# Performance work log

Measured on AMD Instinct MI355X. Metric: run time of the kernel, lower is better.

## Reference

```python
import jax, jax.numpy as jnp
import numpy as np


def setup_inputs() -> dict:
    key = jax.random.key(0)
    ks = jax.random.split(key, 12)
    B, N, Dv, E, H, V, T = 128, 196, 512, 512, 1024, 10000, 20
    s = 0.02  # small init scale for numerical stability
    f = lambda k, shp: (jax.random.normal(k, shp, jnp.float32) * s)
    return {
        "features": jax.random.normal(ks[0], (B, N, Dv), jnp.float32),
        "captions": jax.random.randint(ks[1], (B, T), 0, V),
        "W_init_h": f(ks[2], (H, Dv)),
        "W_init_c": f(ks[3], (H, Dv)),
        "W_attn_v": f(ks[4], (1, Dv)),
        "b_attn_v": jnp.zeros((1,), jnp.float32),
        "W_attn_h": f(ks[5], (1, H)),
        "b_attn_h": jnp.zeros((1,), jnp.float32),
        "embed_table": f(ks[6], (V, E)),
        "W_ih": f(ks[7], (4 * H, Dv + E)),
        "W_hh": f(ks[8], (4 * H, H)),
        "b_ih": jnp.zeros((4 * H,), jnp.float32),
        "b_hh": jnp.zeros((4 * H,), jnp.float32),
        "W_out": f(ks[9], (V, H)),
        "b_out": jnp.zeros((V,), jnp.float32),
    }


def reference(features, captions, W_init_h, W_init_c, W_attn_v, b_attn_v,
              W_attn_h, b_attn_h, embed_table, W_ih, W_hh, b_ih, b_hh,
              W_out, b_out):
    B, N, Dv = features.shape
    # _init_hidden: mean over vis_num of linear projections (division by vis_num)
    h0 = jnp.sum(jnp.einsum('bnd,hd->bnh', features, W_init_h), axis=1) / N
    c0 = jnp.sum(jnp.einsum('bnd,hd->bnh', features, W_init_c), axis=1) / N

    emb = embed_table[captions]                      # B,T,E
    emb_t_major = jnp.swapaxes(emb, 0, 1)            # T,B,E
    # visual attention logits are time-invariant; precompute once
    att_v = jnp.einsum('bnd,od->bno', features, W_attn_v) + b_attn_v  # B,N,1

    def step(carry, emb_t):
        h, c = carry
        # soft attention over vis_num locations
        att_h = (h @ W_attn_h.T + b_attn_h)[:, None, :]   # B,1,1
        alpha = jax.nn.softmax(att_v + att_h, axis=1)     # B,N,1
        ctx = jnp.sum(features * alpha, axis=1)           # B,Dv
        # single-step LSTM (PyTorch gate order: i, f, g, o)
        x = jnp.concatenate([ctx, emb_t], axis=-1)        # B,Dv+E
        gates = x @ W_ih.T + h @ W_hh.T + b_ih + b_hh     # B,4H
        i, fg, g, o = jnp.split(gates, 4, axis=-1)
        c_new = jax.nn.sigmoid(fg) * c + jax.nn.sigmoid(i) * jnp.tanh(g)
        h_new = jax.nn.sigmoid(o) * jnp.tanh(c_new)
        words = h_new @ W_out.T + b_out                   # B,V
        return (h_new, c_new), words

    _, word_space = jax.lax.scan(step, (h0, c0), emb_t_major)  # T,B,V
    # pack_padded_sequence with all-equal lengths flattens time-major -> (T*B, V)
    packed = word_space.reshape(-1, word_space.shape[-1])
    return jax.nn.log_softmax(packed, axis=1), jax.nn.softmax(packed, axis=1)
```

## Files before the change

kernel.cpp:

```cpp
#include <hip/hip_runtime.h>
#include <math.h>

#define B    128
#define NLOC 196
#define DV   512
#define EMB  512
#define HD   1024
#define VV   10000
#define TT   20
#define G4   4096
#define VPAD 10112
#define BH   (B*HD)

typedef short bf16x8 __attribute__((ext_vector_type(8)));
typedef float f32x4  __attribute__((ext_vector_type(4)));

__device__ __forceinline__ unsigned short f2bf(float x) {
    unsigned u = __builtin_bit_cast(unsigned, x);
    unsigned r = (u + 0x7fffu + ((u >> 16) & 1u)) >> 16;
    return (unsigned short)r;
}
__device__ __forceinline__ float bf2f(short s) {
    unsigned u = ((unsigned)(unsigned short)s) << 16;
    return __builtin_bit_cast(float, u);
}

__device__ __forceinline__ void gload_lds16(const void* g, void* lds) {
    __builtin_amdgcn_global_load_lds(
        (const __attribute__((address_space(1))) void*)g,
        (__attribute__((address_space(3))) void*)lds, 16, 0, 0);
}


__global__ void fmean_kernel(const float* __restrict__ feat, short* __restrict__ fmean_b) {
    int idx = blockIdx.x * blockDim.x + threadIdx.x;
    if (idx >= B * DV) return;
    int b = idx / DV, d = idx % DV;
    const float* p = feat + (size_t)b * NLOC * DV + d;
    float s = 0.f;
    for (int n = 0; n < NLOC; ++n) s += p[(size_t)n * DV];
    fmean_b[idx] = (short)f2bf(s * (1.0f / NLOC));
}

__global__ void attv_kernel(const float* __restrict__ feat, const float* __restrict__ wv,
                            const float* __restrict__ bv, float* __restrict__ attv) {
    int row  = blockIdx.x;
    int lane = threadIdx.x;
    const float* p = feat + (size_t)row * DV;
    float s = 0.f;
    for (int k = lane; k < DV; k += 64) s += p[k] * wv[k];
    for (int off = 32; off > 0; off >>= 1) s += __shfl_down(s, off);
    if (lane == 0) attv[row] = s + bv[0];
}

__global__ void alpha_kernel(const float* __restrict__ attv, float* __restrict__ alpha) {
    int b   = blockIdx.x;
    int tid = threadIdx.x;
    __shared__ float red[256];
    float v = (tid < NLOC) ? attv[b * NLOC + tid] : -1e30f;
    red[tid] = v; __syncthreads();
    for (int s = 128; s > 0; s >>= 1) { if (tid < s) red[tid] = fmaxf(red[tid], red[tid + s]); __syncthreads(); }
    float m = red[0]; __syncthreads();
    float e = (tid < NLOC) ? expf(v - m) : 0.f;
    red[tid] = e; __syncthreads();
    for (int s = 128; s > 0; s >>= 1) { if (tid < s) red[tid] += red[tid + s]; __syncthreads(); }
    float sum = red[0];
    if (tid < NLOC) alpha[b * NLOC + tid] = e / sum;
}

__global__ void ctx_kernel(const float* __restrict__ feat, const float* __restrict__ alpha,
                           short* __restrict__ ctx_b) {
    int idx = blockIdx.x * blockDim.x + threadIdx.x;
    if (idx >= B * DV) return;
    int b = idx / DV, d = idx % DV;
    const float* p = feat + (size_t)b * NLOC * DV + d;
    const float* a = alpha + b * NLOC;
    float s = 0.f;
    for (int n = 0; n < NLOC; ++n) s += a[n] * p[(size_t)n * DV];
    ctx_b[idx] = (short)f2bf(s);
}

__global__ void emb_gather_kernel(const int* __restrict__ captions, const float* __restrict__ table,
                                  short* __restrict__ emb_b) {
    size_t idx = (size_t)blockIdx.x * blockDim.x + threadIdx.x;
    if (idx >= (size_t)TT * B * EMB) return;
    int k = (int)(idx % EMB);
    int r = (int)(idx / EMB);
    int t = r / B, b = r % B;
    int cap = captions[b * TT + t];
    emb_b[idx] = (short)f2bf(table[(size_t)cap * EMB + k]);
}

__global__ void f2bf_pad_kernel(const float* __restrict__ in, short* __restrict__ out,
                                size_t n, size_t npad) {
    size_t i = (size_t)blockIdx.x * blockDim.x + threadIdx.x;
    if (i >= npad) return;
    out[i] = (i < n) ? (short)f2bf(in[i]) : (short)0;
}

__global__ void whh_perm_kernel(const float* __restrict__ in, short* __restrict__ out) {
    size_t idx = (size_t)blockIdx.x * blockDim.x + threadIdx.x;
    if (idx >= (size_t)G4 * HD) return;
    int k = (int)(idx & (HD - 1));
    int P = (int)(idx >> 10);
    int u = P >> 2, g = P & 3;
    out[idx] = (short)f2bf(in[(size_t)(g * HD + u) * HD + k]);
}

__global__ void hcvt_kernel(const float* __restrict__ h, short* __restrict__ h_bf) {
    int idx = blockIdx.x * blockDim.x + threadIdx.x;
    if (idx >= B * HD) return;
    h_bf[idx] = (short)f2bf(h[idx]);
}

template<int BN, int WR, int WC, bool BF16OUT>
__global__ __launch_bounds__(256)
void gemm_bf16(const short* __restrict__ A, const short* __restrict__ Bw,
               void* __restrict__ C,
               const float* __restrict__ bias0, const float* __restrict__ bias1,
               int NY, int M, int N, int K, int lda, int ldb, int ldc) {
    constexpr int BM = 128;
    constexpr int BK = 32;
    constexpr int WM = BM / WR;
    constexpr int WN = BN / WC;
    constexpr int FM = WM / 16;
    constexpr int FN = WN / 16;
    __shared__ __align__(16) short As[BM * BK];
    __shared__ __align__(16) short Bs[BN * BK];
    const int tid  = threadIdx.x;
    const int wave = tid >> 6, lane = tid & 63;
    const int wr = wave / WC, wc = wave % WC;

    const int nwg = gridDim.x;
    const int qq = nwg >> 3, rr8 = nwg & 7;
    const int p = blockIdx.x;
    const int xcd = p & 7, slot = p >> 3;
    const int lwg = (xcd < rr8) ? (xcd * (qq + 1) + slot)
                                : (rr8 * (qq + 1) + (xcd - rr8) * qq + slot);
    const int m0 = (lwg % NY) * BM;
    const int n0 = (lwg / NY) * BN;
    const int laneoff = lane * 16;

    f32x4 acc[FM][FN] = {};

    for (int k0 = 0; k0 < K; k0 += BK) {
        #pragma unroll
        for (int r = 0; r < 2; ++r) {
            int o   = r * 4096 + wave * 1024 + laneoff;
            int row = o >> 6;
            int gr  = (o >> 4) & 3;
            int col = ((gr ^ ((row >> 1) & 3)) << 3);
            gload_lds16(A + (size_t)(m0 + row) * lda + k0 + col,
                        (char*)As + r * 4096 + wave * 1024);
        }
        constexpr int BBYTES = BN * BK * 2;
        if constexpr (BBYTES >= 4096) {
            #pragma unroll
            for (int r = 0; r < BBYTES / 4096; ++r) {
                int o   = r * 4096 + wave * 1024 + laneoff;
                int row = o >> 6;
                int gr  = (o >> 4) & 3;
                int col = ((gr ^ ((row >> 1) & 3)) << 3);
                gload_lds16(Bw + (size_t)(n0 + row) * ldb + k0 + col,
                            (char*)Bs + r * 4096 + wave * 1024);
            }
        } else {
            constexpr int NW = BBYTES / 1024;
            if (wave < NW) {
                int o   = wave * 1024 + laneoff;
                int row = o >> 6;
                int gr  = (o >> 4) & 3;
                int col = ((gr ^ ((row >> 1) & 3)) << 3);
                gload_lds16(Bw + (size_t)(n0 + row) * ldb + k0 + col,
                            (char*)Bs + wave * 1024);
            }
        }
        __syncthreads();

        bf16x8 a[FM], b[FN];
        const int kfrg = lane >> 4;
        #pragma unroll
        for (int i = 0; i < FM; ++i) {
            int row = wr * WM + i * 16 + (lane & 15);
            a[i] = *(const bf16x8*)&As[row * BK + ((kfrg ^ ((row >> 1) & 3)) << 3)];
        }
        #pragma unroll
        for (int j = 0; j < FN; ++j) {
            int row = wc * WN + j * 16 + (lane & 15);
            b[j] = *(const bf16x8*)&Bs[row * BK + ((kfrg ^ ((row >> 1) & 3)) << 3)];
        }
        #pragma unroll
        for (int i = 0; i < FM; ++i)
            #pragma unroll
            for (int j = 0; j < FN; ++j)
                acc[i][j] = __builtin_amdgcn_mfma_f32_16x16x32_bf16(a[i], b[j], acc[i][j], 0, 0, 0);
        __syncthreads();
    }

    #pragma unroll
    for (int i = 0; i < FM; ++i) {
        #pragma unroll
        for (int j = 0; j < FN; ++j) {
            int col = n0 + wc * WN + j * 16 + (lane & 15);
            if (col >= N) continue;
            float bv = (bias0 ? bias0[col] : 0.f) + (bias1 ? bias1[col] : 0.f);
            #pragma unroll
            for (int q = 0; q < 4; ++q) {
                int row = m0 + wr * WM + i * 16 + (lane >> 4) * 4 + q;
                if (row < M) {
                    float v = acc[i][j][q] + bv;
                    if constexpr (BF16OUT)
                        ((short*)C)[(size_t)row * ldc + col] = (short)f2bf(v);
                    else
                        ((float*)C)[(size_t)row * ldc + col] = v;
                }
            }
        }
    }
}

__global__ __launch_bounds__(256)
void lstm_step6(const short* __restrict__ Hprev, const short* __restrict__ Whh_p,
                const short* __restrict__ pre_t, const short* __restrict__ gctx_b,
                float* __restrict__ cbuf, short* __restrict__ Hnext,
                short* __restrict__ Hall_t) {
    __shared__ __align__(16) short As[64 * 512];
    __shared__ __align__(16) short Ws[32 * 512];
    __shared__ float gsm[4][64][8];
    const int tid  = threadIdx.x;
    const int lane = tid & 63, wave = tid >> 6;
    const int n0 = blockIdx.x * 32;
    const int m0 = blockIdx.y * 64;

    const int arowL = wave * 16 + (lane & 15);
    const int brow0 = lane & 15;
    const int brow1 = 16 + (lane & 15);
    const int kg    = lane >> 4;

    f32x4 acc0 = {}, acc1 = {};

    for (int h2 = 0; h2 < 2; ++h2) {
        const int k0 = h2 * 512;
        #pragma unroll
        for (int it = 0; it < 16; ++it) {
            int fg  = it * 256 + tid;
            int row = fg >> 6;
            int g   = fg & 63;
            int col = (g ^ (row & 7)) * 8;
            gload_lds16(Hprev + (size_t)(m0 + row) * HD + k0 + col,
                        (char*)As + it * 4096 + wave * 1024);
        }
        #pragma unroll
        for (int it = 0; it < 8; ++it) {
            int fg  = it * 256 + tid;
            int row = fg >> 6;
            int g   = fg & 63;
            int col = (g ^ (row & 7)) * 8;
            gload_lds16(Whh_p + (size_t)(n0 + row) * HD + k0 + col,
                        (char*)Ws + it * 4096 + wave * 1024);
        }
        __syncthreads();
        #pragma unroll
        for (int ks = 0; ks < 16; ++ks) {
            int lg = ks * 4 + kg;
            bf16x8 a  = *(const bf16x8*)((const char*)As + arowL * 1024 + ((lg ^ (arowL & 7)) << 4));
            bf16x8 w0 = *(const bf16x8*)((const char*)Ws + brow0 * 1024 + ((lg ^ (brow0 & 7)) << 4));
            bf16x8 w1 = *(const bf16x8*)((const char*)Ws + brow1 * 1024 + ((lg ^ (brow1 & 7)) << 4));
            acc0 = __builtin_amdgcn_mfma_f32_16x16x32_bf16(a, w0, acc0, 0, 0, 0);
            acc1 = __builtin_amdgcn_mfma_f32_16x16x32_bf16(a, w1, acc1, 0, 0, 0);
        }
        __syncthreads();
    }

    #pragma unroll
    for (int q = 0; q < 4; ++q) {
        int rr = wave * 16 + (lane >> 4) * 4 + q;
        gsm[brow0 & 3][rr][brow0 >> 2] = acc0[q];
        gsm[brow1 & 3][rr][brow1 >> 2] = acc1[q];
    }
    __syncthreads();

    #pragma unroll
    for (int s = 0; s < 2; ++s) {
        int idx = tid + s * 256;
        int m = idx >> 3, u8 = idx & 7;
        int r = m0 + m, u = blockIdx.x * 8 + u8;
        size_t pb = (size_t)r * G4 + u;
        float gi  = gsm[0][m][u8] + bf2f(pre_t[pb])          + bf2f(gctx_b[pb]);
        float gf  = gsm[1][m][u8] + bf2f(pre_t[pb + HD])     + bf2f(gctx_b[pb + HD]);
        float gg2 = gsm[2][m][u8] + bf2f(pre_t[pb + 2 * HD]) + bf2f(gctx_b[pb + 2 * HD]);
        float go  = gsm[3][m][u8] + bf2f(pre_t[pb + 3 * HD]) + bf2f(gctx_b[pb + 3 * HD]);
        float si = 1.f / (1.f + expf(-gi));
        float sf = 1.f / (1.f + expf(-gf));
        float so = 1.f / (1.f + expf(-go));
        float cn = sf * cbuf[(size_t)r * HD + u] + si * tanhf(gg2);
        float hn = so * tanhf(cn);
        cbuf[(size_t)r * HD + u] = cn;
        short hb = (short)f2bf(hn);
        Hnext[(size_t)r * HD + u]  = hb;
        Hall_t[(size_t)r * HD + u] = hb;
    }
}

__global__ __launch_bounds__(512)
void softmax_kernel(const short* __restrict__ wbf, float* __restrict__ logout,
                    float* __restrict__ smout) {
    __shared__ float rowbuf[VV];
    __shared__ float red[512];
    int r = blockIdx.x;
    int tid = threadIdx.x;
    const short* row = wbf + (size_t)r * VV;
    float m = -1e30f;
    for (int i = tid; i < VV; i += 512) {
        float v = bf2f(row[i]);
        rowbuf[i] = v;
        m = fmaxf(m, v);
    }
    red[tid] = m; __syncthreads();
    for (int s = 256; s > 0; s >>= 1) { if (tid < s) red[tid] = fmaxf(red[tid], red[tid + s]); __syncthreads(); }
    m = red[0]; __syncthreads();
    float sum = 0.f;
    for (int i = tid; i < VV; i += 512) sum += expf(rowbuf[i] - m);
    red[tid] = sum; __syncthreads();
    for (int s = 256; s > 0; s >>= 1) { if (tid < s) red[tid] += red[tid + s]; __syncthreads(); }
    sum = red[0];
    float inv = 1.f / sum;
    float lz = logf(sum);
    for (int i = tid; i < VV; i += 512) {
        float x = rowbuf[i];
        smout[(size_t)r * VV + i]  = expf(x - m) * inv;
        logout[(size_t)r * VV + i] = x - m - lz;
    }
}

extern "C" void kernel_launch(void* const* d_in, const int* in_sizes, int n_in,
                              void* d_out, int out_size, void* d_ws, size_t ws_size,
                              hipStream_t stream) {
    const float* features    = (const float*)d_in[0];
    const int*   captions    = (const int*)  d_in[1];
    const float* W_init_h    = (const float*)d_in[2];
    const float* W_init_c    = (const float*)d_in[3];
    const float* W_attn_v    = (const float*)d_in[4];
    const float* b_attn_v    = (const float*)d_in[5];
    const float* embed_table = (const float*)d_in[8];
    const float* W_ih        = (const float*)d_in[9];
    const float* W_hh        = (const float*)d_in[10];
    const float* b_ih        = (const float*)d_in[11];
    const float* b_hh        = (const float*)d_in[12];
    const float* W_out       = (const float*)d_in[13];
    const float* b_out       = (const float*)d_in[14];

    float* out   = (float*)d_out;
    float* words = out;
    float* s2    = out + (size_t)TT * B * VV;

    short* gate_pre_b = (short*)s2;
    short* Hall_b   = (short*)(s2 + (size_t)10485760);
    short* Wout_b   = (short*)(s2 + (size_t)10485760 + 1310720);
    short* Wih_b    = Wout_b + (size_t)VPAD * HD;
    short* Whh_b    = Wih_b  + (size_t)G4 * HD;
    short* Wini_h_b = Whh_b  + (size_t)G4 * HD;
    short* Wini_c_b = Wini_h_b + (size_t)HD * DV;

    char* w = (char*)d_ws;
    size_t off = 0;
    auto alloc = [&](size_t bytes) { void* p = w + off; off = (off + bytes + 255) & ~255UL; return p; };
    float* attv   = (float*)alloc((size_t)B * NLOC * 4);
    float* alpha  = (float*)alloc((size_t)B * NLOC * 4);
    short* gctx_b = (short*)alloc((size_t)B * G4 * 2);
    float* h0f    = (float*)alloc((size_t)B * HD * 4);
    float* cbuf   = (float*)alloc((size_t)B * HD * 4);
    short* fmean_b= (short*)alloc((size_t)B * DV * 2);
    short* ctx_b  = (short*)alloc((size_t)B * DV * 2);
    short* h_ping = (short*)alloc((size_t)B * HD * 2);
    short* h_pong = (short*)alloc((size_t)B * HD * 2);
    short* emb_b  = (short*)alloc((size_t)TT * B * EMB * 2);
    short* words_bf = (short*)alloc((size_t)TT * B * VV * 2);

    f2bf_pad_kernel<<<((size_t)VPAD * HD + 255) / 256, 256, 0, stream>>>(
        W_out, Wout_b, (size_t)VV * HD, (size_t)VPAD * HD);
    f2bf_pad_kernel<<<((size_t)G4 * HD + 255) / 256, 256, 0, stream>>>(
        W_ih, Wih_b, (size_t)G4 * HD, (size_t)G4 * HD);
    whh_perm_kernel<<<((size_t)G4 * HD + 255) / 256, 256, 0, stream>>>(W_hh, Whh_b);
    f2bf_pad_kernel<<<((size_t)HD * DV + 255) / 256, 256, 0, stream>>>(
        W_init_h, Wini_h_b, (size_t)HD * DV, (size_t)HD * DV);
    f2bf_pad_kernel<<<((size_t)HD * DV + 255) / 256, 256, 0, stream>>>(
        W_init_c, Wini_c_b, (size_t)HD * DV, (size_t)HD * DV);

    fmean_kernel<<<(B * DV + 255) / 256, 256, 0, stream>>>(features, fmean_b);
    attv_kernel<<<B * NLOC, 64, 0, stream>>>(features, W_attn_v, b_attn_v, attv);
    alpha_kernel<<<B, 256, 0, stream>>>(attv, alpha);
    ctx_kernel<<<(B * DV + 255) / 256, 256, 0, stream>>>(features, alpha, ctx_b);
    emb_gather_kernel<<<((size_t)TT * B * EMB + 255) / 256, 256, 0, stream>>>(captions, embed_table, emb_b);

    gemm_bf16<32, 4, 1, false><<<dim3(HD / 32), 256, 0, stream>>>(
        fmean_b, Wini_h_b, h0f, nullptr, nullptr, 1, B, HD, DV, DV, DV, HD);
    gemm_bf16<32, 4, 1, false><<<dim3(HD / 32), 256, 0, stream>>>(
        fmean_b, Wini_c_b, cbuf, nullptr, nullptr, 1, B, HD, DV, DV, DV, HD);
    hcvt_kernel<<<(B * HD + 255) / 256, 256, 0, stream>>>(h0f, h_ping);

    gemm_bf16<32, 4, 1, true><<<dim3(G4 / 32), 256, 0, stream>>>(
        ctx_b, Wih_b, gctx_b, b_ih, b_hh, 1, B, G4, DV, DV, HD, G4);
    gemm_bf16<128, 2, 2, true><<<dim3((G4 / 128) * (TT * B / 128)), 256, 0, stream>>>(
        emb_b, Wih_b + DV, gate_pre_b, nullptr, nullptr, TT * B / 128,
        TT * B, G4, EMB, EMB, DV + EMB, G4);

    for (int t = 0; t < TT; ++t) {
        lstm_step6<<<dim3(G4 / 32, B / 64), 256, 0, stream>>>(
            (t & 1) ? h_pong : h_ping, Whh_b, gate_pre_b + (size_t)t * B * G4, gctx_b,
            cbuf, (t & 1) ? h_ping : h_pong, Hall_b + (size_t)t * BH);
    }

    gemm_bf16<128, 2, 2, true><<<dim3((VPAD / 128) * (TT * B / 128)), 256, 0, stream>>>(
        Hall_b, Wout_b, words_bf, b_out, nullptr, TT * B / 128,
        TT * B, VV, HD, HD, HD, VV);
    softmax_kernel<<<TT * B, 512, 0, stream>>>(words_bf, words, s2);
}
```

Measured before the change: 494.1 us.

## Add BK=64 swizzled XCD-aware GEMM and fuse mean/context and h0 conversion

Adds a new GEMM kernel with a K-tile of 64, XOR-swizzled LDS layout and an XCD-aware workgroup remapping. It is used for the embedding-gate GEMM and the big output-projection GEMM. This halves barrier count per K and aims to cut LDS bank conflicts and improve L2 locality across XCDs. It also merges the feature-mean and context reductions into one pass over features, and writes h0 directly in bf16 so the separate conversion kernel is dropped. The new kernel assumes M and N tiles fit the padded buffers, since loads carry no bounds checks.

```diff
diff --git a/kernel.cpp b/kernel.cpp
--- a/kernel.cpp
+++ b/kernel.cpp
@@ -31,16 +31,6 @@
         (__attribute__((address_space(3))) void*)lds, 16, 0, 0);
 }
 
-
-__global__ void fmean_kernel(const float* __restrict__ feat, short* __restrict__ fmean_b) {
-    int idx = blockIdx.x * blockDim.x + threadIdx.x;
-    if (idx >= B * DV) return;
-    int b = idx / DV, d = idx % DV;
-    const float* p = feat + (size_t)b * NLOC * DV + d;
-    float s = 0.f;
-    for (int n = 0; n < NLOC; ++n) s += p[(size_t)n * DV];
-    fmean_b[idx] = (short)f2bf(s * (1.0f / NLOC));
-}
 
 __global__ void attv_kernel(const float* __restrict__ feat, const float* __restrict__ wv,
                             const float* __restrict__ bv, float* __restrict__ attv) {
@@ -68,16 +58,21 @@
     if (tid < NLOC) alpha[b * NLOC + tid] = e / sum;
 }
 
-__global__ void ctx_kernel(const float* __restrict__ feat, const float* __restrict__ alpha,
-                           short* __restrict__ ctx_b) {
+__global__ void fmeanctx_kernel(const float* __restrict__ feat, const float* __restrict__ alpha,
+                                short* __restrict__ fmean_b, short* __restrict__ ctx_b) {
     int idx = blockIdx.x * blockDim.x + threadIdx.x;
     if (idx >= B * DV) return;
     int b = idx / DV, d = idx % DV;
     const float* p = feat + (size_t)b * NLOC * DV + d;
     const float* a = alpha + b * NLOC;
-    float s = 0.f;
-    for (int n = 0; n < NLOC; ++n) s += a[n] * p[(size_t)n * DV];
-    ctx_b[idx] = (short)f2bf(s);
+    float sm = 0.f, sc = 0.f;
+    for (int n = 0; n < NLOC; ++n) {
+        float v = p[(size_t)n * DV];
+        sm += v;
+        sc += a[n] * v;
+    }
+    fmean_b[idx] = (short)f2bf(sm * (1.0f / NLOC));
+    ctx_b[idx]   = (short)f2bf(sc);
 }
 
 __global__ void emb_gather_kernel(const int* __restrict__ captions, const float* __restrict__ table,
@@ -105,12 +100,6 @@
     int P = (int)(idx >> 10);
     int u = P >> 2, g = P & 3;
     out[idx] = (short)f2bf(in[(size_t)(g * HD + u) * HD + k]);
-}
-
-__global__ void hcvt_kernel(const float* __restrict__ h, short* __restrict__ h_bf) {
-    int idx = blockIdx.x * blockDim.x + threadIdx.x;
-    if (idx >= B * HD) return;
-    h_bf[idx] = (short)f2bf(h[idx]);
 }
 
 template<int BN, int WR, int WC, bool BF16OUT>
@@ -214,6 +203,82 @@
                     else
                         ((float*)C)[(size_t)row * ldc + col] = v;
                 }
+            }
+        }
+    }
+}
+
+__global__ __launch_bounds__(256)
+void gemm_k64(const short* __restrict__ A, const short* __restrict__ Bw,
+              short* __restrict__ C,
+              const float* __restrict__ bias0,
+              int NY, int M, int N, int K, int lda, int ldb, int ldc) {
+    __shared__ __align__(16) short As[128 * 64];
+    __shared__ __align__(16) short Bs[128 * 64];
+    const int tid  = threadIdx.x;
+    const int wave = tid >> 6, lane = tid & 63;
+    const int wr = wave >> 1, wc = wave & 1;
+
+    const int nwg = gridDim.x;
+    const int qq = nwg >> 3, rr8 = nwg & 7;
+    const int p = blockIdx.x;
+    const int xcd = p & 7, slot = p >> 3;
+    const int lwg = (xcd < rr8) ? (xcd * (qq + 1) + slot)
+                                : (rr8 * (qq + 1) + (xcd - rr8) * qq + slot);
+    const int m0 = (lwg % NY) * 128;
+    const int n0 = (lwg / NY) * 128;
+    const int laneoff = lane * 16;
+    const int kfrg = lane >> 4;
+
+    f32x4 acc[4][4] = {};
+
+    for (int k0 = 0; k0 < K; k0 += 64) {
+        #pragma unroll
+        for (int r = 0; r < 4; ++r) {
+            int o   = r * 4096 + wave * 1024 + laneoff;
+            int row = o >> 7;
+            int gr  = (o >> 4) & 7;
+            int col = ((gr ^ (row & 7)) << 3);
+            gload_lds16(A + (size_t)(m0 + row) * lda + k0 + col,
+                        (char*)As + r * 4096 + wave * 1024);
+            gload_lds16(Bw + (size_t)(n0 + row) * ldb + k0 + col,
+                        (char*)Bs + r * 4096 + wave * 1024);
+        }
+        __syncthreads();
+
+        #pragma unroll
+        for (int kh = 0; kh < 2; ++kh) {
+            bf16x8 a[4], b[4];
+            #pragma unroll
+            for (int i = 0; i < 4; ++i) {
+                int row = wr * 64 + i * 16 + (lane & 15);
+                a[i] = *(const bf16x8*)&As[row * 64 + (((kh * 4 + kfrg) ^ (row & 7)) << 3)];
+            }
+            #pragma unroll
+            for (int j = 0; j < 4; ++j) {
+                int row = wc * 64 + j * 16 + (lane & 15);
+                b[j] = *(const bf16x8*)&Bs[row * 64 + (((kh * 4 + kfrg) ^ (row & 7)) << 3)];
+            }
+            #pragma unroll
+            for (int i = 0; i < 4; ++i)
+                #pragma unroll
+                for (int j = 0; j < 4; ++j)
+                    acc[i][j] = __builtin_amdgcn_mfma_f32_16x16x32_bf16(a[i], b[j], acc[i][j], 0, 0, 0);
+        }
+        __syncthreads();
+    }
+
+    #pragma unroll
+    for (int i = 0; i < 4; ++i) {
+        #pragma unroll
+        for (int j = 0; j < 4; ++j) {
+            int col = n0 + wc * 64 + j * 16 + (lane & 15);
+            if (col >= N) continue;
+            float bv = bias0 ? bias0[col] : 0.f;
+            #pragma unroll
+            for (int q = 0; q < 4; ++q) {
+                int row = m0 + wr * 64 + i * 16 + (lane >> 4) * 4 + q;
+                if (row < M) C[(size_t)row * ldc + col] = (short)f2bf(acc[i][j][q] + bv);
             }
         }
     }
@@ -368,7 +433,6 @@
     float* attv   = (float*)alloc((size_t)B * NLOC * 4);
     float* alpha  = (float*)alloc((size_t)B * NLOC * 4);
     short* gctx_b = (short*)alloc((size_t)B * G4 * 2);
-    float* h0f    = (float*)alloc((size_t)B * HD * 4);
     float* cbuf   = (float*)alloc((size_t)B * HD * 4);
     short* fmean_b= (short*)alloc((size_t)B * DV * 2);
     short* ctx_b  = (short*)alloc((size_t)B * DV * 2);
@@ -387,22 +451,20 @@
     f2bf_pad_kernel<<<((size_t)HD * DV + 255) / 256, 256, 0, stream>>>(
         W_init_c, Wini_c_b, (size_t)HD * DV, (size_t)HD * DV);
 
-    fmean_kernel<<<(B * DV + 255) / 256, 256, 0, stream>>>(features, fmean_b);
     attv_kernel<<<B * NLOC, 64, 0, stream>>>(features, W_attn_v, b_attn_v, attv);
     alpha_kernel<<<B, 256, 0, stream>>>(attv, alpha);
-    ctx_kernel<<<(B * DV + 255) / 256, 256, 0, stream>>>(features, alpha, ctx_b);
+    fmeanctx_kernel<<<(B * DV + 255) / 256, 256, 0, stream>>>(features, alpha, fmean_b, ctx_b);
     emb_gather_kernel<<<((size_t)TT * B * EMB + 255) / 256, 256, 0, stream>>>(captions, embed_table, emb_b);
 
-    gemm_bf16<32, 4, 1, false><<<dim3(HD / 32), 256, 0, stream>>>(
-        fmean_b, Wini_h_b, h0f, nullptr, nullptr, 1, B, HD, DV, DV, DV, HD);
+    gemm_bf16<32, 4, 1, true><<<dim3(HD / 32), 256, 0, stream>>>(
+        fmean_b, Wini_h_b, h_ping, nullptr, nullptr, 1, B, HD, DV, DV, DV, HD);
     gemm_bf16<32, 4, 1, false><<<dim3(HD / 32), 256, 0, stream>>>(
         fmean_b, Wini_c_b, cbuf, nullptr, nullptr, 1, B, HD, DV, DV, DV, HD);
-    hcvt_kernel<<<(B * HD + 255) / 256, 256, 0, stream>>>(h0f, h_ping);
 
     gemm_bf16<32, 4, 1, true><<<dim3(G4 / 32), 256, 0, stream>>>(
         ctx_b, Wih_b, gctx_b, b_ih, b_hh, 1, B, G4, DV, DV, HD, G4);
-    gemm_bf16<128, 2, 2, true><<<dim3((G4 / 128) * (TT * B / 128)), 256, 0, stream>>>(
-        emb_b, Wih_b + DV, gate_pre_b, nullptr, nullptr, TT * B / 128,
+    gemm_k64<<<dim3((G4 / 128) * (TT * B / 128)), 256, 0, stream>>>(
+        emb_b, Wih_b + DV, gate_pre_b, nullptr, TT * B / 128,
         TT * B, G4, EMB, EMB, DV + EMB, G4);
 
     for (int t = 0; t < TT; ++t) {
@@ -411,8 +473,8 @@
             cbuf, (t & 1) ? h_ping : h_pong, Hall_b + (size_t)t * BH);
     }
 
-    gemm_bf16<128, 2, 2, true><<<dim3((VPAD / 128) * (TT * B / 128)), 256, 0, stream>>>(
-        Hall_b, Wout_b, words_bf, b_out, nullptr, TT * B / 128,
+    gemm_k64<<<dim3((VPAD / 128) * (TT * B / 128)), 256, 0, stream>>>(
+        Hall_b, Wout_b, words_bf, b_out, TT * B / 128,
         TT * B, VV, HD, HD, HD, VV);
     softmax_kernel<<<TT * B, 512, 0, stream>>>(words_bf, words, s2);
 }
```

After: 485.9 us. About the same (-1.7%).
